# Kernel tuning notes

Hardware: AMD Instinct MI355X
Metric: run time of the kernel (lower is better)

Reference implementation:

```python
import jax, jax.numpy as jnp
import numpy as np

D = 768          # TGLU_hidden_dim == input_hidden_dim
E = 8            # num_experts
TOP_K = 2        # top_experts
N_ENT = 32       # num_entity
B = 16           # batch (mentions)
L = 128          # max_seq_len
EPS = 1e-5


def setup_inputs() -> dict:
    key = jax.random.key(0)
    ks = jax.random.split(key, 16)
    s = 0.02
    return {
        "entity_text_cls": jax.random.normal(ks[0], (N_ENT, D), jnp.float32),
        "entity_text_tokens": jax.random.normal(ks[1], (N_ENT, L, D), jnp.float32),
        "mention_text_cls": jax.random.normal(ks[2], (B, D), jnp.float32),
        "mention_text_tokens": jax.random.normal(ks[3], (B, L, D), jnp.float32),
        # SwitchMoE params: gate + per-expert Linear(dim -> output_dim)
        "gate_w": jax.random.normal(ks[4], (D, E), jnp.float32) * s,
        "gate_b": jnp.zeros((E,), jnp.float32),
        "exp_w": jax.random.normal(ks[5], (E, D, D), jnp.float32) * s,
        "exp_b": jnp.zeros((E, D), jnp.float32),
        # attention projections
        "wq": jax.random.normal(ks[6], (D, D), jnp.float32) * s,
        "bq": jnp.zeros((D,), jnp.float32),
        "wk": jax.random.normal(ks[7], (D, D), jnp.float32) * s,
        "bk": jnp.zeros((D,), jnp.float32),
        "wv": jax.random.normal(ks[8], (D, D), jnp.float32) * s,
        "bv": jnp.zeros((D,), jnp.float32),
        # LayerNorm params
        "ln_w": jnp.ones((D,), jnp.float32),
        "ln_b": jnp.zeros((D,), jnp.float32),
    }


def _switch_moe(x, gate_w, gate_b, exp_w, exp_b):
    # x: [n, s, D] -> [n, s, D]; top-k router, renormalized combine.
    logits = jnp.einsum("nsd,de->nse", x, gate_w) + gate_b
    probs = jax.nn.softmax(logits, axis=-1)
    vals, idx = jax.lax.top_k(probs, TOP_K)              # [n,s,k]
    vals = vals / jnp.sum(vals, axis=-1, keepdims=True)
    # combine weights over all experts (zero for unselected) -> dense mask form
    w = jnp.sum(jax.nn.one_hot(idx, E, dtype=x.dtype) * vals[..., None], axis=-2)  # [n,s,E]
    eo = jnp.einsum("nsd,edo->nseo", x, exp_w) + exp_b   # [n,s,E,D]
    return jnp.einsum("nse,nseo->nso", w, eo)


def _layernorm(x, w, b):
    mu = jnp.mean(x, axis=-1, keepdims=True)
    var = jnp.mean(jnp.square(x - mu), axis=-1, keepdims=True)
    return (x - mu) * jax.lax.rsqrt(var + EPS) * w + b


def reference(entity_text_cls, entity_text_tokens, mention_text_cls, mention_text_tokens,
              gate_w, gate_b, exp_w, exp_b, wq, bq, wk, bk, wv, bv, ln_w, ln_b):
    # prepend CLS, route through shared MoE
    ent = jnp.concatenate([entity_text_cls[:, None, :], entity_text_tokens], axis=1)   # [N,L+1,D]
    ent_moe = _switch_moe(ent, gate_w, gate_b, exp_w, exp_b)
    ent_cls_moe = ent_moe[:, 0, :]          # [N,D]
    ent_tok = ent_moe[:, 1:, :]             # [N,L,D]

    men = jnp.concatenate([mention_text_cls[:, None, :], mention_text_tokens], axis=1)  # [B,L+1,D]
    men_moe = _switch_moe(men, gate_w, gate_b, exp_w, exp_b)
    men_tok = men_moe[:, 1:, :]             # [B,L,D]

    q = jnp.einsum("nld,do->nlo", ent_tok, wq) + bq    # [N,L,D]
    k = jnp.einsum("bmd,do->bmo", men_tok, wk) + bk    # [B,L,D]
    v = jnp.einsum("bmd,do->bmo", men_tok, wv) + bv    # [B,L,D]

    # all-pairs entity x mention cross attention: [N,B,L,L]
    scores = jnp.einsum("nld,bmd->nblm", q, k) / jnp.sqrt(jnp.asarray(D, q.dtype))
    probs = jax.nn.softmax(scores, axis=-1)
    context = jnp.einsum("nblm,bmd->nbld", probs, v)   # [N,B,L,D]
    context = jnp.mean(context, axis=-2)               # [N,B,D]
    context = _layernorm(context, ln_w, ln_b)

    g2l = jnp.sum(ent_cls_moe[:, None, :] * context, axis=-1)   # [N,B]
    g2l = g2l.T                                                  # [B,N]
    g2g = mention_text_cls @ entity_text_cls.T                   # [B,N]
    return (g2l + g2g) / 2
```

## Files before the change

### kernel.cpp

```cpp
#include <hip/hip_runtime.h>
#include <math.h>

#define D 768
#define NE 8
#define NTOK 6192
#define MEN_TOK0 4128

typedef __attribute__((ext_vector_type(8))) short short8;
typedef __attribute__((ext_vector_type(4))) short short4b;
typedef __attribute__((ext_vector_type(4))) float floatx4;

__device__ __forceinline__ short f2bf(float f) {
  union { float f; unsigned u; } x; x.f = f;
  unsigned r = x.u + 0x7fffu + ((x.u >> 16) & 1u);
  return (short)(r >> 16);
}
__device__ __forceinline__ float bf2f(short s) {
  union { unsigned u; float f; } x; x.u = ((unsigned)(unsigned short)s) << 16;
  return x.f;
}

__device__ __forceinline__ void gload16(const short* g, short8* lds_base) {
  __builtin_amdgcn_global_load_lds(
      (const __attribute__((address_space(1))) unsigned int*)g,
      (__attribute__((address_space(3))) unsigned int*)lds_base,
      16, 0, 0);
}

__device__ __forceinline__ const float* token_row(int t,
    const float* __restrict__ ecls, const float* __restrict__ etok,
    const float* __restrict__ mcls, const float* __restrict__ mtok) {
  if (t < MEN_TOK0) {
    int n = t / 129, s = t - n * 129;
    return (s == 0) ? (ecls + n * D) : (etok + (size_t)(n * 128 + s - 1) * D);
  } else {
    int tm = t - MEN_TOK0;
    int b = tm / 129, s = tm - b * 129;
    return (s == 0) ? (mcls + b * D) : (mtok + (size_t)(b * 128 + s - 1) * D);
  }
}

__global__ __launch_bounds__(256) void prep_kernel(
    const float* __restrict__ ecls, const float* __restrict__ etok,
    const float* __restrict__ mcls, const float* __restrict__ mtok,
    const float* __restrict__ gate_w, const float* __restrict__ gate_b,
    const float* __restrict__ exp_w, const float* __restrict__ wq,
    const float* __restrict__ wk, const float* __restrict__ wv,
    int* __restrict__ te1, int* __restrict__ te2,
    float* __restrict__ tw1, float* __restrict__ tw2,
    short* __restrict__ Xb, short* __restrict__ expwT, short* __restrict__ wT) {
  __shared__ float tbuf[64][65];
  int bid = blockIdx.x;
  int tid = threadIdx.x;
  if (bid < 1548) {
    int t = bid * 4 + (tid >> 6);
    int lane = tid & 63;
    const float* xr = token_row(t, ecls, etok, mcls, mtok);
    float acc[NE];
#pragma unroll
    for (int e = 0; e < NE; ++e) acc[e] = 0.f;
#pragma unroll
    for (int it = 0; it < 3; ++it) {
      int d0 = lane * 4 + it * 256;
      floatx4 x = *(const floatx4*)(xr + d0);
      short4b xb;
#pragma unroll
      for (int q = 0; q < 4; ++q) {
        xb[q] = f2bf(x[q]);
        float xv = x[q];
#pragma unroll
        for (int e = 0; e < NE; ++e) acc[e] += xv * gate_w[(d0 + q) * NE + e];
      }
      *(short4b*)(Xb + (size_t)t * D + d0) = xb;
    }
#pragma unroll
    for (int e = 0; e < NE; ++e) {
#pragma unroll
      for (int off = 32; off > 0; off >>= 1) acc[e] += __shfl_down(acc[e], off);
    }
    if (lane == 0) {
      float lg[NE];
#pragma unroll
      for (int e = 0; e < NE; ++e) lg[e] = acc[e] + gate_b[e];
      int e1 = 0;
#pragma unroll
      for (int e = 1; e < NE; ++e) if (lg[e] > lg[e1]) e1 = e;
      int e2 = (e1 == 0) ? 1 : 0;
#pragma unroll
      for (int e = 0; e < NE; ++e) {
        if (e != e1 && lg[e] > lg[e2]) e2 = e;
      }
      float w1 = 1.f / (1.f + __expf(lg[e2] - lg[e1]));
      te1[t] = e1; te2[t] = e2;
      tw1[t] = w1; tw2[t] = 1.f - w1;
    }
  } else {
    int zz = bid - 1548;
    int z = zz / 144, rem = zz % 144;
    int k0 = (rem / 12) * 64, o0 = (rem % 12) * 64;
    const float* src; short* dst;
    if (z < 8) { src = exp_w + (size_t)z * D * D; dst = expwT + (size_t)z * D * D; }
    else { src = (z == 8) ? wq : (z == 9) ? wk : wv; dst = wT + (size_t)(z - 8) * D * D; }
    int tx = tid & 63, ty = tid >> 6;
#pragma unroll
    for (int i = 0; i < 16; ++i) {
      int k = i * 4 + ty;
      tbuf[k][tx] = src[(size_t)(k0 + k) * D + o0 + tx];
    }
    __syncthreads();
#pragma unroll
    for (int i = 0; i < 16; ++i) {
      int o = i * 4 + ty;
      dst[(size_t)(o0 + o) * D + k0 + tx] = f2bf(tbuf[tx][o]);
    }
  }
}

__global__ __launch_bounds__(1024) void route_kernel(
    const int* __restrict__ te1, const int* __restrict__ te2,
    int* __restrict__ lst_tok, int* __restrict__ slot1, int* __restrict__ slot2,
    int* __restrict__ cnt, int* __restrict__ basee) {
  __shared__ int hist[NE];
  __shared__ int base_s[NE];
  int tid = threadIdx.x;
  if (tid < NE) hist[tid] = 0;
  __syncthreads();
  for (int t = tid; t < NTOK; t += 1024) {
    atomicAdd(&hist[te1[t]], 1);
    atomicAdd(&hist[te2[t]], 1);
  }
  __syncthreads();
  if (tid == 0) {
    int acc = 0;
    for (int e = 0; e < NE; ++e) {
      base_s[e] = acc;
      cnt[e] = hist[e];
      basee[e] = acc;
      acc += hist[e];
    }
  }
  __syncthreads();
  if (tid < NE) hist[tid] = 0;
  __syncthreads();
  for (int t = tid; t < NTOK; t += 1024) {
    int e1 = te1[t], e2 = te2[t];
    int r1 = atomicAdd(&hist[e1], 1);
    int r2 = atomicAdd(&hist[e2], 1);
    int s1 = base_s[e1] + r1;
    int s2 = base_s[e2] + r2;
    slot1[t] = s1; slot2[t] = s2;
    lst_tok[s1] = t; lst_tok[s2] = t;
  }
}

__global__ __launch_bounds__(256, 4) void moe_kernel(
    const short* __restrict__ Xb, const short* __restrict__ expwT,
    const int* __restrict__ cnt, const int* __restrict__ basee,
    const int* __restrict__ lst_tok, short* __restrict__ EO) {
  int id = blockIdx.x;
  int e = id & 7;
  int r = id >> 3;
  int ob = r % 6;
  int tb = r / 6;
  int count = cnt[e];
  int t0 = tb * 128;
  if (t0 >= count) return;
  int o0 = ob * 128;
  int gb = basee[e];

  __shared__ short8 As[1024];
  __shared__ short8 Bs[1024];
  __shared__ int stok[128];

  int tid = threadIdx.x;
  int l = tid & 63, w = tid >> 6;
  int wr = w >> 1, wc = w & 1;

  if (tid < 128) {
    int p = t0 + tid;
    stok[tid] = lst_tok[gb + (p < count ? p : 0)];
  }
  __syncthreads();

  const short* Bg = expwT + (size_t)e * D * D;
  const short* srcA[2];
  const short* srcB[2];
#pragma unroll
  for (int q = 0; q < 2; ++q) {
    int s = (q << 8) + (w << 6) + l;
    int row = s >> 2, cc = s & 3;
    int csrc = (cc ^ ((row >> 1) & 3)) * 8;
    srcA[q] = Xb + (size_t)stok[row] * D + csrc;
    srcB[q] = Bg + (size_t)(o0 + row) * D + csrc;
  }

  floatx4 acc[4][4];
#pragma unroll
  for (int ai = 0; ai < 4; ++ai)
#pragma unroll
    for (int bj = 0; bj < 4; ++bj) acc[ai][bj] = (floatx4){0.f, 0.f, 0.f, 0.f};

#pragma unroll
  for (int q = 0; q < 2; ++q) {
    gload16(srcA[q], &As[(q << 8) + (w << 6)]);
    gload16(srcB[q], &Bs[(q << 8) + (w << 6)]);
  }
  __syncthreads();

  for (int it = 0; it < 24; ++it) {
    int cur = (it & 1) << 9;
    if (it < 23) {
      int nxt = cur ^ 512;
      int k0n = (it + 1) * 32;
#pragma unroll
      for (int q = 0; q < 2; ++q) {
        gload16(srcA[q] + k0n, &As[nxt + (q << 8) + (w << 6)]);
        gload16(srcB[q] + k0n, &Bs[nxt + (q << 8) + (w << 6)]);
      }
    }
    int kc = l >> 4;
    short8 a[4], bb[4];
#pragma unroll
    for (int ai = 0; ai < 4; ++ai) {
      int ar = wr * 64 + ai * 16 + (l & 15);
      a[ai] = As[cur + (ar << 2) + (kc ^ ((ar >> 1) & 3))];
    }
#pragma unroll
    for (int bj = 0; bj < 4; ++bj) {
      int br = wc * 64 + bj * 16 + (l & 15);
      bb[bj] = Bs[cur + (br << 2) + (kc ^ ((br >> 1) & 3))];
    }
#pragma unroll
    for (int ai = 0; ai < 4; ++ai)
#pragma unroll
      for (int bj = 0; bj < 4; ++bj)
        acc[ai][bj] = __builtin_amdgcn_mfma_f32_16x16x32_bf16(a[ai], bb[bj], acc[ai][bj], 0, 0, 0);
    __syncthreads();
  }

#pragma unroll
  for (int ai = 0; ai < 4; ++ai) {
#pragma unroll
    for (int rr = 0; rr < 4; ++rr) {
      int rowl = wr * 64 + ai * 16 + ((l >> 4) << 2) + rr;
      int p = t0 + rowl;
      if (p < count) {
        size_t off = (size_t)(gb + p) * D;
#pragma unroll
        for (int bj = 0; bj < 4; ++bj) {
          int col = o0 + wc * 64 + bj * 16 + (l & 15);
          EO[off + col] = f2bf(acc[ai][bj][rr]);
        }
      }
    }
  }
}

__global__ __launch_bounds__(256) void combine_kernel(
    const short* __restrict__ EO,
    const int* __restrict__ te1, const int* __restrict__ te2,
    const float* __restrict__ tw1, const float* __restrict__ tw2,
    const int* __restrict__ slot1, const int* __restrict__ slot2,
    const float* __restrict__ exp_b, short* __restrict__ MOEb) {
  int idx = blockIdx.x * 256 + threadIdx.x;
  int t = idx / 96, cg = idx - t * 96;
  int c0 = cg * 8;
  int e1 = te1[t], e2 = te2[t];
  float w1 = tw1[t], w2 = tw2[t];
  short8 a = *(const short8*)(EO + (size_t)slot1[t] * D + c0);
  short8 b = *(const short8*)(EO + (size_t)slot2[t] * D + c0);
  const float* b1 = exp_b + e1 * D + c0;
  const float* b2 = exp_b + e2 * D + c0;
  short8 o;
#pragma unroll
  for (int j = 0; j < 8; ++j)
    o[j] = f2bf(w1 * (bf2f(a[j]) + b1[j]) + w2 * (bf2f(b[j]) + b2[j]));
  *(short8*)(MOEb + (size_t)t * D + c0) = o;
}

__global__ __launch_bounds__(256, 6) void qkv_kernel(
    const short* __restrict__ MOEb, const short* __restrict__ wT,
    const float* __restrict__ bq, const float* __restrict__ bk,
    const float* __restrict__ bv,
    short* __restrict__ Qb, short* __restrict__ Kb, short* __restrict__ Vb) {
  int id = blockIdx.x;
  int z, r;
  if (id < 384)      { z = 0; r = id; }
  else if (id < 576) { z = 1; r = id - 384; }
  else               { z = 2; r = id - 576; }
  int tb = r / 6, ob = r % 6;
  int o0 = ob * 128;
  int base = (z == 0) ? 0 : MEN_TOK0;
  const short* W = wT + (size_t)z * D * D;
  const float* bias = (z == 0) ? bq : (z == 1) ? bk : bv;
  int tokbase = base + (tb >> 1) * 129 + 1 + (tb & 1) * 64;
  const short* Ag = MOEb + (size_t)tokbase * D;

  __shared__ short8 As[512];
  __shared__ short8 Bs[1024];

  int tid = threadIdx.x;
  int l = tid & 63, w = tid >> 6;
  int wr = w >> 1, wc = w & 1;

  const short* srcA;
  const short* srcB[2];
  {
    int s = tid;
    int row = s >> 2, cc = s & 3;
    int csrc = (cc ^ ((row >> 1) & 3)) * 8;
    srcA = Ag + (size_t)row * D + csrc;
  }
#pragma unroll
  for (int q = 0; q < 2; ++q) {
    int s = (q << 8) + tid;
    int row = s >> 2, cc = s & 3;
    int csrc = (cc ^ ((row >> 1) & 3)) * 8;
    srcB[q] = W + (size_t)(o0 + row) * D + csrc;
  }

  floatx4 acc[2][4];
#pragma unroll
  for (int ai = 0; ai < 2; ++ai)
#pragma unroll
    for (int bj = 0; bj < 4; ++bj) acc[ai][bj] = (floatx4){0.f, 0.f, 0.f, 0.f};

  gload16(srcA, &As[w << 6]);
#pragma unroll
  for (int q = 0; q < 2; ++q) gload16(srcB[q], &Bs[(q << 8) + (w << 6)]);
  __syncthreads();

  for (int it = 0; it < 24; ++it) {
    int curA = (it & 1) << 8;
    int curB = (it & 1) << 9;
    if (it < 23) {
      int k0n = (it + 1) * 32;
      gload16(srcA + k0n, &As[(curA ^ 256) + (w << 6)]);
#pragma unroll
      for (int q = 0; q < 2; ++q)
        gload16(srcB[q] + k0n, &Bs[(curB ^ 512) + (q << 8) + (w << 6)]);
    }
    int kc = l >> 4;
    short8 a[2], bb[4];
#pragma unroll
    for (int ai = 0; ai < 2; ++ai) {
      int ar = wr * 32 + ai * 16 + (l & 15);
      a[ai] = As[curA + (ar << 2) + (kc ^ ((ar >> 1) & 3))];
    }
#pragma unroll
    for (int bj = 0; bj < 4; ++bj) {
      int br = wc * 64 + bj * 16 + (l & 15);
      bb[bj] = Bs[curB + (br << 2) + (kc ^ ((br >> 1) & 3))];
    }
#pragma unroll
    for (int ai = 0; ai < 2; ++ai)
#pragma unroll
      for (int bj = 0; bj < 4; ++bj)
        acc[ai][bj] = __builtin_amdgcn_mfma_f32_16x16x32_bf16(a[ai], bb[bj], acc[ai][bj], 0, 0, 0);
    __syncthreads();
  }

#pragma unroll
  for (int ai = 0; ai < 2; ++ai) {
#pragma unroll
    for (int rr = 0; rr < 4; ++rr) {
      int rowl = wr * 32 + ai * 16 + ((l >> 4) << 2) + rr;
      size_t rglob = (size_t)tb * 64 + rowl;
#pragma unroll
      for (int bj = 0; bj < 4; ++bj) {
        int col = o0 + wc * 64 + bj * 16 + (l & 15);
        float v = acc[ai][bj][rr] + bias[col];
        if (z == 0)      Qb[rglob * D + col] = f2bf(v);
        else if (z == 1) Kb[rglob * D + col] = f2bf(v);
        else             Vb[rglob * D + col] = f2bf(v);
      }
    }
  }
}

__device__ __forceinline__ float blockSum(float v, volatile float* red, int tid) {
#pragma unroll
  for (int off = 32; off > 0; off >>= 1) v += __shfl_down(v, off);
  __syncthreads();
  if ((tid & 63) == 0) red[tid >> 6] = v;
  __syncthreads();
  return red[0] + red[1] + red[2] + red[3];
}

__global__ __launch_bounds__(256, 4) void attn_kernel(
    const short* __restrict__ Qb, const short* __restrict__ Kb,
    const short* __restrict__ Vb, const short* __restrict__ MOEb,
    const float* __restrict__ ecls, const float* __restrict__ mcls,
    const float* __restrict__ ln_w, const float* __restrict__ ln_b,
    float* __restrict__ out) {
  int id = blockIdx.x;
  int n = id & 31, b = id >> 5;
  __shared__ short8 Qs[1024];
  __shared__ short8 Ks[1024];
  __shared__ float pb[128];
  __shared__ float red[4];
  int tid = threadIdx.x;
  int l = tid & 63, w = tid >> 6;
  if (tid < 128) pb[tid] = 0.f;

  floatx4 acc[2][8];
#pragma unroll
  for (int i = 0; i < 2; ++i)
#pragma unroll
    for (int j = 0; j < 8; ++j) acc[i][j] = (floatx4){0.f, 0.f, 0.f, 0.f};

  const short* qg = Qb + (size_t)n * 128 * D;
  const short* kg = Kb + (size_t)b * 128 * D;

  const short* srcQ[2];
  const short* srcK[2];
#pragma unroll
  for (int q = 0; q < 2; ++q) {
    int s = (q << 8) + tid;
    int row = s >> 2, cc = s & 3;
    int csrc = (cc ^ ((row >> 1) & 3)) * 8;
    srcQ[q] = qg + (size_t)row * D + csrc;
    srcK[q] = kg + (size_t)row * D + csrc;
  }

#pragma unroll
  for (int q = 0; q < 2; ++q) {
    gload16(srcQ[q], &Qs[(q << 8) + (w << 6)]);
    gload16(srcK[q], &Ks[(q << 8) + (w << 6)]);
  }
  __syncthreads();

  for (int it = 0; it < 24; ++it) {
    int cur = (it & 1) << 9;
    if (it < 23) {
      int nxt = cur ^ 512;
      int k0n = (it + 1) * 32;
#pragma unroll
      for (int q = 0; q < 2; ++q) {
        gload16(srcQ[q] + k0n, &Qs[nxt + (q << 8) + (w << 6)]);
        gload16(srcK[q] + k0n, &Ks[nxt + (q << 8) + (w << 6)]);
      }
    }
    int kc = l >> 4;
    short8 a[2], bb[8];
#pragma unroll
    for (int i = 0; i < 2; ++i) {
      int ar = w * 32 + i * 16 + (l & 15);
      a[i] = Qs[cur + (ar << 2) + (kc ^ ((ar >> 1) & 3))];
    }
#pragma unroll
    for (int j = 0; j < 8; ++j) {
      int br = j * 16 + (l & 15);
      bb[j] = Ks[cur + (br << 2) + (kc ^ ((br >> 1) & 3))];
    }
#pragma unroll
    for (int i = 0; i < 2; ++i)
#pragma unroll
      for (int j = 0; j < 8; ++j)
        acc[i][j] = __builtin_amdgcn_mfma_f32_16x16x32_bf16(a[i], bb[j], acc[i][j], 0, 0, 0);
    __syncthreads();
  }

  const float scale = 0.03608439182435161f;
  float colsum[8];
#pragma unroll
  for (int j = 0; j < 8; ++j) colsum[j] = 0.f;

#pragma unroll
  for (int i = 0; i < 2; ++i) {
#pragma unroll
    for (int r = 0; r < 4; ++r) {
      float mx = -3.0e38f;
#pragma unroll
      for (int j = 0; j < 8; ++j) mx = fmaxf(mx, acc[i][j][r]);
      mx = fmaxf(mx, __shfl_xor(mx, 1));
      mx = fmaxf(mx, __shfl_xor(mx, 2));
      mx = fmaxf(mx, __shfl_xor(mx, 4));
      mx = fmaxf(mx, __shfl_xor(mx, 8));
      float pv[8], sm = 0.f;
#pragma unroll
      for (int j = 0; j < 8; ++j) { pv[j] = __expf((acc[i][j][r] - mx) * scale); sm += pv[j]; }
      sm += __shfl_xor(sm, 1);
      sm += __shfl_xor(sm, 2);
      sm += __shfl_xor(sm, 4);
      sm += __shfl_xor(sm, 8);
      float inv = 1.f / sm;
#pragma unroll
      for (int j = 0; j < 8; ++j) colsum[j] += pv[j] * inv;
    }
  }
#pragma unroll
  for (int j = 0; j < 8; ++j) {
    colsum[j] += __shfl_xor(colsum[j], 16);
    colsum[j] += __shfl_xor(colsum[j], 32);
  }
  if (l < 16) {
#pragma unroll
    for (int j = 0; j < 8; ++j) atomicAdd(&pb[j * 16 + l], colsum[j]);
  }
  __syncthreads();

  float ctx[3];
  const short* vb = Vb + (size_t)b * 128 * D;
#pragma unroll
  for (int rp = 0; rp < 3; ++rp) {
    int d = tid + rp * 256;
    float a = 0.f;
    for (int m = 0; m < 128; ++m) a += pb[m] * bf2f(vb[(size_t)m * D + d]);
    ctx[rp] = a * (1.f / 128.f);
  }

  float mu = blockSum(ctx[0] + ctx[1] + ctx[2], red, tid) * (1.f / 768.f);
  float vs = 0.f;
#pragma unroll
  for (int rp = 0; rp < 3; ++rp) { float c = ctx[rp] - mu; vs += c * c; }
  float var = blockSum(vs, red, tid) * (1.f / 768.f);
  float rstd = rsqrtf(var + 1e-5f);

  const short* em = MOEb + (size_t)(n * 129) * D;
  float g2l_p = 0.f, g2g_p = 0.f;
#pragma unroll
  for (int rp = 0; rp < 3; ++rp) {
    int d = tid + rp * 256;
    float cl = (ctx[rp] - mu) * rstd * ln_w[d] + ln_b[d];
    g2l_p += bf2f(em[d]) * cl;
    g2g_p += mcls[(size_t)b * D + d] * ecls[(size_t)n * D + d];
  }
  float g2l = blockSum(g2l_p, red, tid);
  float g2g = blockSum(g2g_p, red, tid);
  if (tid == 0) out[b * 32 + n] = 0.5f * (g2l + g2g);
}

extern "C" void kernel_launch(void* const* d_in, const int* in_sizes, int n_in,
                              void* d_out, int out_size, void* d_ws, size_t ws_size,
                              hipStream_t stream) {
  const float* ecls   = (const float*)d_in[0];
  const float* etok   = (const float*)d_in[1];
  const float* mcls   = (const float*)d_in[2];
  const float* mtok   = (const float*)d_in[3];
  const float* gate_w = (const float*)d_in[4];
  const float* gate_b = (const float*)d_in[5];
  const float* exp_w  = (const float*)d_in[6];
  const float* exp_b  = (const float*)d_in[7];
  const float* wq     = (const float*)d_in[8];
  const float* bq     = (const float*)d_in[9];
  const float* wk     = (const float*)d_in[10];
  const float* bk     = (const float*)d_in[11];
  const float* wv     = (const float*)d_in[12];
  const float* bv     = (const float*)d_in[13];
  const float* ln_w   = (const float*)d_in[14];
  const float* ln_b   = (const float*)d_in[15];
  float* outp = (float*)d_out;

  char* ws = (char*)d_ws;
  short* Qb    = (short*)(ws + 0);
  short* Kb    = (short*)(ws + 6291456);
  short* Vb    = (short*)(ws + 9437184);
  short* Xb    = (short*)(ws + 12582912);
  short* EO    = (short*)(ws + 22093824);
  short* MOEb  = (short*)(ws + 41115648);
  short* expwT = (short*)(ws + 50626560);
  short* wT    = (short*)(ws + 60063744);
  int*   te1   = (int*)  (ws + 63602688);
  int*   te2   = (int*)  (ws + 63627456);
  float* tw1   = (float*)(ws + 63652224);
  float* tw2   = (float*)(ws + 63676992);
  int*   slot1 = (int*)  (ws + 63701760);
  int*   slot2 = (int*)  (ws + 63726528);
  int*   lst_tok = (int*)(ws + 63751296);
  int*   cnt   = (int*)  (ws + 63800832);
  int*   basee = (int*)  (ws + 63800864);

  prep_kernel<<<1548 + 1584, 256, 0, stream>>>(ecls, etok, mcls, mtok, gate_w, gate_b,
                                               exp_w, wq, wk, wv,
                                               te1, te2, tw1, tw2, Xb, expwT, wT);
  route_kernel<<<1, 1024, 0, stream>>>(te1, te2, lst_tok, slot1, slot2, cnt, basee);
  moe_kernel<<<49 * 6 * 8, 256, 0, stream>>>(Xb, expwT, cnt, basee, lst_tok, EO);
  combine_kernel<<<2322, 256, 0, stream>>>(EO, te1, te2, tw1, tw2, slot1, slot2,
                                           exp_b, MOEb);
  qkv_kernel<<<768, 256, 0, stream>>>(MOEb, wT, bq, bk, bv, Qb, Kb, Vb);
  attn_kernel<<<512, 256, 0, stream>>>(Qb, Kb, Vb, MOEb, ecls, mcls, ln_w, ln_b, outp);
}
```

Measured before the change: 133.6 us.

## Double threads per block in MoE, QKV and attention GEMM kernels

Moves the three MFMA kernels from 256 to 512 threads (8 waves) per block. Each wave now owns a smaller slice of the output tile, so it holds fewer accumulators, and each thread issues one async global-to-LDS load per operand instead of two. The attention epilogue is rewritten to compute the context and LayerNorm with 512 threads, using a new 8-wave block reduction. The aim is more waves for latency hiding and lower register pressure per thread, at the cost of more barrier overhead and fewer MFMAs per LDS fragment read.

```diff
diff --git a/kernel.cpp b/kernel.cpp
--- a/kernel.cpp
+++ b/kernel.cpp
@@ -153,7 +153,7 @@
   }
 }
 
-__global__ __launch_bounds__(256, 4) void moe_kernel(
+__global__ __launch_bounds__(512, 4) void moe_kernel(
     const short* __restrict__ Xb, const short* __restrict__ expwT,
     const int* __restrict__ cnt, const int* __restrict__ basee,
     const int* __restrict__ lst_tok, short* __restrict__ EO) {
@@ -183,46 +183,33 @@
   __syncthreads();
 
   const short* Bg = expwT + (size_t)e * D * D;
-  const short* srcA[2];
-  const short* srcB[2];
-#pragma unroll
-  for (int q = 0; q < 2; ++q) {
-    int s = (q << 8) + (w << 6) + l;
-    int row = s >> 2, cc = s & 3;
-    int csrc = (cc ^ ((row >> 1) & 3)) * 8;
-    srcA[q] = Xb + (size_t)stok[row] * D + csrc;
-    srcB[q] = Bg + (size_t)(o0 + row) * D + csrc;
-  }
-
-  floatx4 acc[4][4];
-#pragma unroll
-  for (int ai = 0; ai < 4; ++ai)
+  int srow = tid >> 2, scc = tid & 3;
+  int csrc = (scc ^ ((srow >> 1) & 3)) * 8;
+  const short* srcA = Xb + (size_t)stok[srow] * D + csrc;
+  const short* srcB = Bg + (size_t)(o0 + srow) * D + csrc;
+
+  floatx4 acc[2][4];
+#pragma unroll
+  for (int ai = 0; ai < 2; ++ai)
 #pragma unroll
     for (int bj = 0; bj < 4; ++bj) acc[ai][bj] = (floatx4){0.f, 0.f, 0.f, 0.f};
 
-#pragma unroll
-  for (int q = 0; q < 2; ++q) {
-    gload16(srcA[q], &As[(q << 8) + (w << 6)]);
-    gload16(srcB[q], &Bs[(q << 8) + (w << 6)]);
-  }
+  gload16(srcA, &As[w << 6]);
+  gload16(srcB, &Bs[w << 6]);
   __syncthreads();
 
   for (int it = 0; it < 24; ++it) {
     int cur = (it & 1) << 9;
     if (it < 23) {
-      int nxt = cur ^ 512;
       int k0n = (it + 1) * 32;
-#pragma unroll
-      for (int q = 0; q < 2; ++q) {
-        gload16(srcA[q] + k0n, &As[nxt + (q << 8) + (w << 6)]);
-        gload16(srcB[q] + k0n, &Bs[nxt + (q << 8) + (w << 6)]);
-      }
+      gload16(srcA + k0n, &As[(cur ^ 512) + (w << 6)]);
+      gload16(srcB + k0n, &Bs[(cur ^ 512) + (w << 6)]);
     }
     int kc = l >> 4;
-    short8 a[4], bb[4];
-#pragma unroll
-    for (int ai = 0; ai < 4; ++ai) {
-      int ar = wr * 64 + ai * 16 + (l & 15);
+    short8 a[2], bb[4];
+#pragma unroll
+    for (int ai = 0; ai < 2; ++ai) {
+      int ar = wr * 32 + ai * 16 + (l & 15);
       a[ai] = As[cur + (ar << 2) + (kc ^ ((ar >> 1) & 3))];
     }
 #pragma unroll
@@ -231,7 +218,7 @@
       bb[bj] = Bs[cur + (br << 2) + (kc ^ ((br >> 1) & 3))];
     }
 #pragma unroll
-    for (int ai = 0; ai < 4; ++ai)
+    for (int ai = 0; ai < 2; ++ai)
 #pragma unroll
       for (int bj = 0; bj < 4; ++bj)
         acc[ai][bj] = __builtin_amdgcn_mfma_f32_16x16x32_bf16(a[ai], bb[bj], acc[ai][bj], 0, 0, 0);
@@ -239,10 +226,10 @@
   }
 
 #pragma unroll
-  for (int ai = 0; ai < 4; ++ai) {
+  for (int ai = 0; ai < 2; ++ai) {
 #pragma unroll
     for (int rr = 0; rr < 4; ++rr) {
-      int rowl = wr * 64 + ai * 16 + ((l >> 4) << 2) + rr;
+      int rowl = wr * 32 + ai * 16 + ((l >> 4) << 2) + rr;
       int p = t0 + rowl;
       if (p < count) {
         size_t off = (size_t)(gb + p) * D;
@@ -278,7 +265,7 @@
   *(short8*)(MOEb + (size_t)t * D + c0) = o;
 }
 
-__global__ __launch_bounds__(256, 6) void qkv_kernel(
+__global__ __launch_bounds__(512, 4) void qkv_kernel(
     const short* __restrict__ MOEb, const short* __restrict__ wT,
     const float* __restrict__ bq, const float* __restrict__ bk,
     const float* __restrict__ bv,
@@ -303,31 +290,17 @@
   int l = tid & 63, w = tid >> 6;
   int wr = w >> 1, wc = w & 1;
 
-  const short* srcA;
-  const short* srcB[2];
-  {
-    int s = tid;
-    int row = s >> 2, cc = s & 3;
-    int csrc = (cc ^ ((row >> 1) & 3)) * 8;
-    srcA = Ag + (size_t)row * D + csrc;
-  }
-#pragma unroll
-  for (int q = 0; q < 2; ++q) {
-    int s = (q << 8) + tid;
-    int row = s >> 2, cc = s & 3;
-    int csrc = (cc ^ ((row >> 1) & 3)) * 8;
-    srcB[q] = W + (size_t)(o0 + row) * D + csrc;
-  }
-
-  floatx4 acc[2][4];
-#pragma unroll
-  for (int ai = 0; ai < 2; ++ai)
-#pragma unroll
-    for (int bj = 0; bj < 4; ++bj) acc[ai][bj] = (floatx4){0.f, 0.f, 0.f, 0.f};
-
-  gload16(srcA, &As[w << 6]);
-#pragma unroll
-  for (int q = 0; q < 2; ++q) gload16(srcB[q], &Bs[(q << 8) + (w << 6)]);
+  int srow = tid >> 2, scc = tid & 3;
+  int csrc = (scc ^ ((srow >> 1) & 3)) * 8;
+  const short* srcA = Ag + (size_t)(srow & 63) * D + csrc;
+  const short* srcB = W + (size_t)(o0 + srow) * D + csrc;
+
+  floatx4 acc[4];
+#pragma unroll
+  for (int bj = 0; bj < 4; ++bj) acc[bj] = (floatx4){0.f, 0.f, 0.f, 0.f};
+
+  if (w < 4) gload16(srcA, &As[w << 6]);
+  gload16(srcB, &Bs[w << 6]);
   __syncthreads();
 
   for (int it = 0; it < 24; ++it) {
@@ -335,59 +308,52 @@
     int curB = (it & 1) << 9;
     if (it < 23) {
       int k0n = (it + 1) * 32;
-      gload16(srcA + k0n, &As[(curA ^ 256) + (w << 6)]);
-#pragma unroll
-      for (int q = 0; q < 2; ++q)
-        gload16(srcB[q] + k0n, &Bs[(curB ^ 512) + (q << 8) + (w << 6)]);
+      if (w < 4) gload16(srcA + k0n, &As[(curA ^ 256) + (w << 6)]);
+      gload16(srcB + k0n, &Bs[(curB ^ 512) + (w << 6)]);
     }
     int kc = l >> 4;
-    short8 a[2], bb[4];
-#pragma unroll
-    for (int ai = 0; ai < 2; ++ai) {
-      int ar = wr * 32 + ai * 16 + (l & 15);
-      a[ai] = As[curA + (ar << 2) + (kc ^ ((ar >> 1) & 3))];
-    }
+    int ar = wr * 16 + (l & 15);
+    short8 a = As[curA + (ar << 2) + (kc ^ ((ar >> 1) & 3))];
+    short8 bb[4];
 #pragma unroll
     for (int bj = 0; bj < 4; ++bj) {
       int br = wc * 64 + bj * 16 + (l & 15);
       bb[bj] = Bs[curB + (br << 2) + (kc ^ ((br >> 1) & 3))];
     }
 #pragma unroll
-    for (int ai = 0; ai < 2; ++ai)
-#pragma unroll
-      for (int bj = 0; bj < 4; ++bj)
-        acc[ai][bj] = __builtin_amdgcn_mfma_f32_16x16x32_bf16(a[ai], bb[bj], acc[ai][bj], 0, 0, 0);
+    for (int bj = 0; bj < 4; ++bj)
+      acc[bj] = __builtin_amdgcn_mfma_f32_16x16x32_bf16(a, bb[bj], acc[bj], 0, 0, 0);
     __syncthreads();
   }
 
 #pragma unroll
-  for (int ai = 0; ai < 2; ++ai) {
-#pragma unroll
-    for (int rr = 0; rr < 4; ++rr) {
-      int rowl = wr * 32 + ai * 16 + ((l >> 4) << 2) + rr;
-      size_t rglob = (size_t)tb * 64 + rowl;
-#pragma unroll
-      for (int bj = 0; bj < 4; ++bj) {
-        int col = o0 + wc * 64 + bj * 16 + (l & 15);
-        float v = acc[ai][bj][rr] + bias[col];
-        if (z == 0)      Qb[rglob * D + col] = f2bf(v);
-        else if (z == 1) Kb[rglob * D + col] = f2bf(v);
-        else             Vb[rglob * D + col] = f2bf(v);
-      }
-    }
-  }
-}
-
-__device__ __forceinline__ float blockSum(float v, volatile float* red, int tid) {
+  for (int rr = 0; rr < 4; ++rr) {
+    int rowl = wr * 16 + ((l >> 4) << 2) + rr;
+    size_t rglob = (size_t)tb * 64 + rowl;
+#pragma unroll
+    for (int bj = 0; bj < 4; ++bj) {
+      int col = o0 + wc * 64 + bj * 16 + (l & 15);
+      float v = acc[bj][rr] + bias[col];
+      if (z == 0)      Qb[rglob * D + col] = f2bf(v);
+      else if (z == 1) Kb[rglob * D + col] = f2bf(v);
+      else             Vb[rglob * D + col] = f2bf(v);
+    }
+  }
+}
+
+__device__ __forceinline__ float blockSum512(float v, volatile float* red, int tid) {
 #pragma unroll
   for (int off = 32; off > 0; off >>= 1) v += __shfl_down(v, off);
   __syncthreads();
   if ((tid & 63) == 0) red[tid >> 6] = v;
   __syncthreads();
-  return red[0] + red[1] + red[2] + red[3];
-}
-
-__global__ __launch_bounds__(256, 4) void attn_kernel(
+  float s = 0.f;
+#pragma unroll
+  for (int i = 0; i < 8; ++i) s += red[i];
+  return s;
+}
+
+__global__ __launch_bounds__(512, 4) void attn_kernel(
     const short* __restrict__ Qb, const short* __restrict__ Kb,
     const short* __restrict__ Vb, const short* __restrict__ MOEb,
     const float* __restrict__ ecls, const float* __restrict__ mcls,
@@ -398,66 +364,46 @@
   __shared__ short8 Qs[1024];
   __shared__ short8 Ks[1024];
   __shared__ float pb[128];
-  __shared__ float red[4];
+  __shared__ float red[8];
   int tid = threadIdx.x;
   int l = tid & 63, w = tid >> 6;
   if (tid < 128) pb[tid] = 0.f;
 
-  floatx4 acc[2][8];
-#pragma unroll
-  for (int i = 0; i < 2; ++i)
-#pragma unroll
-    for (int j = 0; j < 8; ++j) acc[i][j] = (floatx4){0.f, 0.f, 0.f, 0.f};
+  floatx4 acc[8];
+#pragma unroll
+  for (int j = 0; j < 8; ++j) acc[j] = (floatx4){0.f, 0.f, 0.f, 0.f};
 
   const short* qg = Qb + (size_t)n * 128 * D;
   const short* kg = Kb + (size_t)b * 128 * D;
 
-  const short* srcQ[2];
-  const short* srcK[2];
-#pragma unroll
-  for (int q = 0; q < 2; ++q) {
-    int s = (q << 8) + tid;
-    int row = s >> 2, cc = s & 3;
-    int csrc = (cc ^ ((row >> 1) & 3)) * 8;
-    srcQ[q] = qg + (size_t)row * D + csrc;
-    srcK[q] = kg + (size_t)row * D + csrc;
-  }
-
-#pragma unroll
-  for (int q = 0; q < 2; ++q) {
-    gload16(srcQ[q], &Qs[(q << 8) + (w << 6)]);
-    gload16(srcK[q], &Ks[(q << 8) + (w << 6)]);
-  }
+  int srow = tid >> 2, scc = tid & 3;
+  int csrc = (scc ^ ((srow >> 1) & 3)) * 8;
+  const short* srcQ = qg + (size_t)srow * D + csrc;
+  const short* srcK = kg + (size_t)srow * D + csrc;
+
+  gload16(srcQ, &Qs[w << 6]);
+  gload16(srcK, &Ks[w << 6]);
   __syncthreads();
 
   for (int it = 0; it < 24; ++it) {
     int cur = (it & 1) << 9;
     if (it < 23) {
-      int nxt = cur ^ 512;
       int k0n = (it + 1) * 32;
-#pragma unroll
-      for (int q = 0; q < 2; ++q) {
-        gload16(srcQ[q] + k0n, &Qs[nxt + (q << 8) + (w << 6)]);
-        gload16(srcK[q] + k0n, &Ks[nxt + (q << 8) + (w << 6)]);
-      }
+      gload16(srcQ + k0n, &Qs[(cur ^ 512) + (w << 6)]);
+      gload16(srcK + k0n, &Ks[(cur ^ 512) + (w << 6)]);
     }
     int kc = l >> 4;
-    short8 a[2], bb[8];
-#pragma unroll
-    for (int i = 0; i < 2; ++i) {
-      int ar = w * 32 + i * 16 + (l & 15);
-      a[i] = Qs[cur + (ar << 2) + (kc ^ ((ar >> 1) & 3))];
-    }
+    int ar = w * 16 + (l & 15);
+    short8 a = Qs[cur + (ar << 2) + (kc ^ ((ar >> 1) & 3))];
+    short8 bb[8];
 #pragma unroll
     for (int j = 0; j < 8; ++j) {
       int br = j * 16 + (l & 15);
       bb[j] = Ks[cur + (br << 2) + (kc ^ ((br >> 1) & 3))];
     }
 #pragma unroll
-    for (int i = 0; i < 2; ++i)
-#pragma unroll
-      for (int j = 0; j < 8; ++j)
-        acc[i][j] = __builtin_amdgcn_mfma_f32_16x16x32_bf16(a[i], bb[j], acc[i][j], 0, 0, 0);
+    for (int j = 0; j < 8; ++j)
+      acc[j] = __builtin_amdgcn_mfma_f32_16x16x32_bf16(a, bb[j], acc[j], 0, 0, 0);
     __syncthreads();
   }
 
@@ -467,27 +413,24 @@
   for (int j = 0; j < 8; ++j) colsum[j] = 0.f;
 
 #pragma unroll
-  for (int i = 0; i < 2; ++i) {
-#pragma unroll
-    for (int r = 0; r < 4; ++r) {
-      float mx = -3.0e38f;
-#pragma unroll
-      for (int j = 0; j < 8; ++j) mx = fmaxf(mx, acc[i][j][r]);
-      mx = fmaxf(mx, __shfl_xor(mx, 1));
-      mx = fmaxf(mx, __shfl_xor(mx, 2));
-      mx = fmaxf(mx, __shfl_xor(mx, 4));
-      mx = fmaxf(mx, __shfl_xor(mx, 8));
-      float pv[8], sm = 0.f;
-#pragma unroll
-      for (int j = 0; j < 8; ++j) { pv[j] = __expf((acc[i][j][r] - mx) * scale); sm += pv[j]; }
-      sm += __shfl_xor(sm, 1);
-      sm += __shfl_xor(sm, 2);
-      sm += __shfl_xor(sm, 4);
-      sm += __shfl_xor(sm, 8);
-      float inv = 1.f / sm;
-#pragma unroll
-      for (int j = 0; j < 8; ++j) colsum[j] += pv[j] * inv;
-    }
+  for (int r = 0; r < 4; ++r) {
+    float mx = -3.0e38f;
+#pragma unroll
+    for (int j = 0; j < 8; ++j) mx = fmaxf(mx, acc[j][r]);
+    mx = fmaxf(mx, __shfl_xor(mx, 1));
+    mx = fmaxf(mx, __shfl_xor(mx, 2));
+    mx = fmaxf(mx, __shfl_xor(mx, 4));
+    mx = fmaxf(mx, __shfl_xor(mx, 8));
+    float pv[8], sm = 0.f;
+#pragma unroll
+    for (int j = 0; j < 8; ++j) { pv[j] = __expf((acc[j][r] - mx) * scale); sm += pv[j]; }
+    sm += __shfl_xor(sm, 1);
+    sm += __shfl_xor(sm, 2);
+    sm += __shfl_xor(sm, 4);
+    sm += __shfl_xor(sm, 8);
+    float inv = 1.f / sm;
+#pragma unroll
+    for (int j = 0; j < 8; ++j) colsum[j] += pv[j] * inv;
   }
 #pragma unroll
   for (int j = 0; j < 8; ++j) {
@@ -500,34 +443,33 @@
   }
   __syncthreads();
 
-  float ctx[3];
+  int d2 = (tid & 255) + 512;
+  float ctx0 = 0.f, ctx1 = 0.f;
   const short* vb = Vb + (size_t)b * 128 * D;
-#pragma unroll
-  for (int rp = 0; rp < 3; ++rp) {
-    int d = tid + rp * 256;
-    float a = 0.f;
-    for (int m = 0; m < 128; ++m) a += pb[m] * bf2f(vb[(size_t)m * D + d]);
-    ctx[rp] = a * (1.f / 128.f);
-  }
-
-  float mu = blockSum(ctx[0] + ctx[1] + ctx[2], red, tid) * (1.f / 768.f);
-  float vs = 0.f;
-#pragma unroll
-  for (int rp = 0; rp < 3; ++rp) { float c = ctx[rp] - mu; vs += c * c; }
-  float var = blockSum(vs, red, tid) * (1.f / 768.f);
+  for (int m = 0; m < 128; ++m) {
+    float p = pb[m];
+    const short* row = vb + (size_t)m * D;
+    ctx0 += p * bf2f(row[tid]);
+    ctx1 += p * bf2f(row[d2]);
+  }
+  ctx0 *= (1.f / 128.f);
+  ctx1 *= (1.f / 128.f);
+  bool lo = tid < 256;
+
+  float mu = blockSum512(ctx0 + (lo ? ctx1 : 0.f), red, tid) * (1.f / 768.f);
+  float c0 = ctx0 - mu, c1 = ctx1 - mu;
+  float vs = c0 * c0 + (lo ? c1 * c1 : 0.f);
+  float var = blockSum512(vs, red, tid) * (1.f / 768.f);
   float rstd = rsqrtf(var + 1e-5f);
 
   const short* em = MOEb + (size_t)(n * 129) * D;
-  float g2l_p = 0.f, g2g_p = 0.f;
-#pragma unroll
-  for (int rp = 0; rp < 3; ++rp) {
-    int d = tid + rp * 256;
-    float cl = (ctx[rp] - mu) * rstd * ln_w[d] + ln_b[d];
-    g2l_p += bf2f(em[d]) * cl;
-    g2g_p += mcls[(size_t)b * D + d] * ecls[(size_t)n * D + d];
-  }
-  float g2l = blockSum(g2l_p, red, tid);
-  float g2g = blockSum(g2g_p, red, tid);
+  float cl0 = c0 * rstd * ln_w[tid] + ln_b[tid];
+  float cl1 = c1 * rstd * ln_w[d2] + ln_b[d2];
+  float g2l_p = bf2f(em[tid]) * cl0 + (lo ? bf2f(em[d2]) * cl1 : 0.f);
+  float g2g_p = mcls[(size_t)b * D + tid] * ecls[(size_t)n * D + tid] +
+                (lo ? mcls[(size_t)b * D + d2] * ecls[(size_t)n * D + d2] : 0.f);
+  float g2l = blockSum512(g2l_p, red, tid);
+  float g2g = blockSum512(g2g_p, red, tid);
   if (tid == 0) out[b * 32 + n] = 0.5f * (g2l + g2g);
 }
 
@@ -575,9 +517,9 @@
                                                exp_w, wq, wk, wv,
                                                te1, te2, tw1, tw2, Xb, expwT, wT);
   route_kernel<<<1, 1024, 0, stream>>>(te1, te2, lst_tok, slot1, slot2, cnt, basee);
-  moe_kernel<<<49 * 6 * 8, 256, 0, stream>>>(Xb, expwT, cnt, basee, lst_tok, EO);
+  moe_kernel<<<49 * 6 * 8, 512, 0, stream>>>(Xb, expwT, cnt, basee, lst_tok, EO);
   combine_kernel<<<2322, 256, 0, stream>>>(EO, te1, te2, tw1, tw2, slot1, slot2,
                                            exp_b, MOEb);
-  qkv_kernel<<<768, 256, 0, stream>>>(MOEb, wT, bq, bk, bv, Qb, Kb, Vb);
-  attn_kernel<<<512, 256, 0, stream>>>(Qb, Kb, Vb, MOEb, ecls, mcls, ln_w, ln_b, outp);
-}
+  qkv_kernel<<<768, 512, 0, stream>>>(MOEb, wT, bq, bk, bv, Qb, Kb, Vb);
+  attn_kernel<<<512, 512, 0, stream>>>(Qb, Kb, Vb, MOEb, ecls, mcls, ln_w, ln_b, outp);
+}
```

Measured after the change: 124.9 us. -6.5%, faster.
